# Optimization experiments

Hardware: AMD Instinct MI355X
Metric: run time of the kernel (lower is better)

## Reference

```python
import jax, jax.numpy as jnp
import numpy as np

HEADS = 4

def _layernorm(x, g, b, eps=1e-5):
    mu = x.mean(-1, keepdims=True)
    var = ((x - mu) ** 2).mean(-1, keepdims=True)
    return (x - mu) / jnp.sqrt(var + eps) * g + b

def _feature_map(data, proj, is_query, eps=1e-4):
    # FAVOR+ softmax kernel features. data: [B,H,S,dh], proj: [m,dh]
    dh = data.shape[-1]
    m = proj.shape[0]
    dn = dh ** -0.25
    ratio = m ** -0.5
    dash = jnp.einsum('bhsd,md->bhsm', data * dn, proj)
    diag = 0.5 * jnp.sum((data * dn) ** 2, axis=-1, keepdims=True)
    mx = jnp.max(dash, axis=-1, keepdims=True) if is_query else jnp.max(dash)
    return ratio * (jnp.exp(dash - diag - mx) + eps)

def _causal_linear_attention(q, k, v):
    # q,k: [B,H,S,m] kernel features; v: [B,H,S,dh]
    k_cum = jnp.cumsum(k, axis=2)                                  # [B,H,S,m]
    d_inv = 1.0 / jnp.einsum('bhsm,bhsm->bhs', q, k_cum)           # [B,H,S]
    ctx = jnp.cumsum(jnp.einsum('bhsm,bhsd->bhsmd', k, v), axis=2) # [B,H,S,m,dh]
    return jnp.einsum('bhsmd,bhsm,bhs->bhsd', ctx, q, d_inv)

def reference(x, pre_w, pre_b, ln1_g, ln1_b, wq, wk, wv, wo, bo, proj,
              ln2_g, ln2_b, ff_w1, ff_b1, ff_w2, ff_b2, tgt_w, tgt_b, rd_w, rd_b):
    # preproc: 1x1x1 conv3d + softplus
    xbn = jax.nn.softplus(jnp.einsum('bcthw,oc->bothw', x, pre_w)
                          + pre_b[None, :, None, None, None])
    B, D, T, H, W = xbn.shape
    tokens = xbn.reshape(B, -1, D)  # raw torch-style reshape, S = T*H*W
    S = tokens.shape[1]

    # Performer block (depth=1): prenorm attention + prenorm FF, residuals
    h = _layernorm(tokens, ln1_g, ln1_b)
    split = lambda t: t.reshape(B, S, HEADS, -1).transpose(0, 2, 1, 3)
    q, k, v = split(h @ wq), split(h @ wk), split(h @ wv)
    qp = _feature_map(q, proj, True)
    kp = _feature_map(k, proj, False)
    attn = _causal_linear_attention(qp, kp, v)
    attn = attn.transpose(0, 2, 1, 3).reshape(B, S, D)
    tokens = tokens + attn @ wo + bo
    h2 = _layernorm(tokens, ln2_g, ln2_b)
    tokens = tokens + jax.nn.gelu(h2 @ ff_w1 + ff_b1, approximate=False) @ ff_w2 + ff_b2

    # readout
    out = tokens.reshape(B, D, T, H, W).mean(axis=2)               # [B,D,H,W]
    out = jnp.concatenate([out, x[:, 2, 0][:, None]], axis=1)      # [B,D+1,H,W]
    out = jax.lax.conv_general_dilated(out, tgt_w, (1, 1), [(2, 2), (2, 2)],
                                       dimension_numbers=('NCHW', 'OIHW', 'NCHW'))
    out = out + tgt_b[None, :, None, None]
    out = out.mean(axis=(2, 3))                                    # global avg pool -> [B,1]
    return out @ rd_w.T + rd_b


def setup_inputs() -> dict:
    key = jax.random.key(0)
    ks = jax.random.split(key, 12)
    B, T, H, W = 2, 8, 48, 48
    D, DH, M, FF = 64, 16, 32, 256
    s = lambda k, shape, sc=1.0: jax.random.normal(k, shape, jnp.float32) * sc
    inv = 1.0 / np.sqrt(D)
    return {
        'x': s(ks[0], (B, 3, T, H, W)),
        'pre_w': s(ks[1], (D, 3), 1.0 / np.sqrt(3)),
        'pre_b': jnp.zeros((D,), jnp.float32),
        'ln1_g': jnp.ones((D,), jnp.float32), 'ln1_b': jnp.zeros((D,), jnp.float32),
        'wq': s(ks[2], (D, D), inv), 'wk': s(ks[3], (D, D), inv), 'wv': s(ks[4], (D, D), inv),
        'wo': s(ks[5], (D, D), inv), 'bo': jnp.zeros((D,), jnp.float32),
        'proj': s(ks[6], (M, DH)),
        'ln2_g': jnp.ones((D,), jnp.float32), 'ln2_b': jnp.zeros((D,), jnp.float32),
        'ff_w1': s(ks[7], (D, FF), inv), 'ff_b1': jnp.zeros((FF,), jnp.float32),
        'ff_w2': s(ks[8], (FF, D), 1.0 / np.sqrt(FF)), 'ff_b2': jnp.zeros((D,), jnp.float32),
        'tgt_w': s(ks[9], (1, D + 1, 5, 5), 1.0 / np.sqrt((D + 1) * 25)),
        'tgt_b': jnp.zeros((1,), jnp.float32),
        'rd_w': s(ks[10], (1, 1)), 'rd_b': jnp.zeros((1,), jnp.float32),
    }
```

## Files before the change

### kernel.cpp

```cpp
#include <hip/hip_runtime.h>
#include <hip/hip_bf16.h>
#include <math.h>

typedef __hip_bfloat16 bf16;
typedef __attribute__((ext_vector_type(8))) short short8;
typedef __attribute__((ext_vector_type(16))) float floatx16;

constexpr int B_   = 2;
constexpr int T_   = 8;
constexpr int HW   = 48 * 48;
constexpr int S_   = T_ * HW;
constexpr int D_   = 64;
constexpr int NH   = 4;
constexpr int DH   = 16;
constexpr int M_   = 32;
constexpr int BS   = B_ * S_;
constexpr int BSD  = BS * D_;
constexpr int BH   = B_ * NH;
constexpr int BHS  = BH * S_;
constexpr int CHUNK = 32;
constexpr int NC   = S_ / CHUNK;
constexpr int STATE = M_ * DH + M_;
constexpr int GSLOTS = 64;
constexpr int GSTRIDE = 32;
constexpr int SRG = 16;
constexpr int SRUN = NC / SRG;
constexpr int SCB = 16;
constexpr float DN = 0.5f;
constexpr float RATIO = 0.17677669529663687f;

__device__ __forceinline__ unsigned short f2bf(float f) {
  bf16 h = __float2bfloat16(f);
  return *reinterpret_cast<unsigned short*>(&h);
}
__device__ __forceinline__ float bf2f(bf16 v) { return __bfloat162float(v); }
__device__ __forceinline__ float bfs2f(short s) {
  return __uint_as_float(((unsigned)(unsigned short)s) << 16);
}
__device__ __forceinline__ void atomicMaxFloat(float* addr, float val) {
  if (val >= 0.f) atomicMax((int*)addr, __float_as_int(val));
  else atomicMin((unsigned int*)addr, __float_as_uint(val));
}

__global__ void __launch_bounds__(256) k_prep(const float* __restrict__ wq,
        const float* __restrict__ wk, const float* __restrict__ wv,
        const float* __restrict__ wo, const float* __restrict__ w1,
        const float* __restrict__ proj,
        short* __restrict__ wqT, short* __restrict__ wkT, short* __restrict__ wvT,
        short* __restrict__ woT, short* __restrict__ w1T, short* __restrict__ projb,
        float* __restrict__ gmax) {
  int tid = blockIdx.x * 256 + threadIdx.x;
  if (tid < GSLOTS) ((unsigned*)gmax)[tid * GSTRIDE] = 0xff800000u;
  if (tid < 512) projb[tid] = (short)f2bf(proj[tid]);
  if (tid < 4096) {
    int c = tid >> 6, r = tid & 63;
    wqT[tid] = (short)f2bf(wq[r * 64 + c]);
    wkT[tid] = (short)f2bf(wk[r * 64 + c]);
    wvT[tid] = (short)f2bf(wv[r * 64 + c]);
    woT[tid] = (short)f2bf(wo[r * 64 + c]);
  }
  {
    int c = tid >> 6, r = tid & 63;
    w1T[tid] = (short)f2bf(w1[r * 256 + c]);
  }
}

__global__ void __launch_bounds__(256) k_preqkv(const float* __restrict__ x,
                      const float* __restrict__ pw, const float* __restrict__ pb,
                      const float* __restrict__ g, const float* __restrict__ bb,
                      const short* __restrict__ wqT, const short* __restrict__ wkT,
                      const short* __restrict__ wvT, const short* __restrict__ projb,
                      bf16* __restrict__ tok, bf16* __restrict__ q,
                      bf16* __restrict__ k, bf16* __restrict__ v,
                      float* __restrict__ gmax) {
  __shared__ __align__(16) short sh[32 * 64];
  __shared__ __align__(16) short sk[32 * 64];
  int tid = threadIdx.x;
  int tbase = blockIdx.x * 32;

  {
    size_t f0 = (size_t)tbase * 64;
    int b = (int)(f0 / ((size_t)D_ * S_));
    int rem = (int)(f0 % ((size_t)D_ * S_));
    int d = rem / S_;
    int pos0 = rem % S_;
    float w0 = pw[d * 3 + 0], w1 = pw[d * 3 + 1], w2 = pw[d * 3 + 2], pbd = pb[d];
    const float* xb = x + ((size_t)b * 3) * S_ + pos0 + tid * 8;
    float4 x0a = *(const float4*)(xb);
    float4 x0b = *(const float4*)(xb + 4);
    float4 x1a = *(const float4*)(xb + S_);
    float4 x1b = *(const float4*)(xb + S_ + 4);
    float4 x2a = *(const float4*)(xb + 2 * S_);
    float4 x2b = *(const float4*)(xb + 2 * S_ + 4);
    float xf0[8] = {x0a.x, x0a.y, x0a.z, x0a.w, x0b.x, x0b.y, x0b.z, x0b.w};
    float xf1[8] = {x1a.x, x1a.y, x1a.z, x1a.w, x1b.x, x1b.y, x1b.z, x1b.w};
    float xf2[8] = {x2a.x, x2a.y, x2a.z, x2a.w, x2b.x, x2b.y, x2b.z, x2b.w};
    float t[8];
    short8 tv;
#pragma unroll
    for (int j = 0; j < 8; ++j) {
      float a = xf0[j] * w0 + xf1[j] * w1 + xf2[j] * w2 + pbd;
      t[j] = fmaxf(a, 0.f) + log1pf(expf(-fabsf(a)));
      tv[j] = (short)f2bf(t[j]);
    }
    *(short8*)(tok + f0 + (size_t)tid * 8) = tv;
    float s1 = 0.f, s2 = 0.f;
#pragma unroll
    for (int j = 0; j < 8; ++j) { s1 += t[j]; s2 += t[j] * t[j]; }
#pragma unroll
    for (int off = 4; off; off >>= 1) {
      s1 += __shfl_xor(s1, off, 8);
      s2 += __shfl_xor(s2, off, 8);
    }
    float mu = s1 * (1.f / 64.f);
    float var = s2 * (1.f / 64.f) - mu * mu;
    float rs = rsqrtf(var + 1e-5f);
    int tt = tid >> 3, j8 = tid & 7;
    short8 hv;
#pragma unroll
    for (int j = 0; j < 8; ++j) {
      int c = j8 * 8 + j;
      hv[j] = (short)f2bf((t[j] - mu) * rs * g[c] + bb[c]);
    }
    *(short8*)&sh[tt * 64 + ((j8 ^ (tt & 7)) * 8)] = hv;
  }
  __syncthreads();

  int w = tid >> 6;
  int L = tid & 63;
  int half = L >> 5;
  int n = L & 31;

  if (w < 3) {
    const short* wmT = (w == 0) ? wqT : (w == 1) ? wkT : wvT;
    bf16* outm = (w == 0) ? q : (w == 1) ? k : v;

    short8 a[4];
#pragma unroll
    for (int c = 0; c < 4; ++c)
      a[c] = *(const short8*)&sh[n * 64 + (((c * 2 + half) ^ (n & 7)) * 8)];
#pragma unroll
    for (int ct = 0; ct < 2; ++ct) {
      int col = ct * 32 + n;
      short8 bfrag[4];
#pragma unroll
      for (int c = 0; c < 4; ++c)
        bfrag[c] = *(const short8*)&wmT[col * 64 + c * 16 + half * 8];
      floatx16 acc;
#pragma unroll
      for (int i = 0; i < 16; ++i) acc[i] = 0.f;
      acc = __builtin_amdgcn_mfma_f32_32x32x16_bf16(a[0], bfrag[0], acc, 0, 0, 0);
      acc = __builtin_amdgcn_mfma_f32_32x32x16_bf16(a[1], bfrag[1], acc, 0, 0, 0);
      acc = __builtin_amdgcn_mfma_f32_32x32x16_bf16(a[2], bfrag[2], acc, 0, 0, 0);
      acc = __builtin_amdgcn_mfma_f32_32x32x16_bf16(a[3], bfrag[3], acc, 0, 0, 0);
      int head = col >> 4, di = col & 15;
#pragma unroll
      for (int r = 0; r < 16; ++r) {
        int row = (r & 3) + 8 * (r >> 2) + 4 * half;
        int token = tbase + row;
        int b = token / S_, s = token % S_;
        unsigned short us = f2bf(acc[r]);
        if (w == 2) {
          outm[((size_t)(b * NH + head) * S_ + s) * DH + di] = *(bf16*)&us;
        } else {
          unsigned short usd = f2bf(bfs2f((short)us) * DN);
          outm[((size_t)(b * NH + head) * S_ + s) * DH + di] = *(bf16*)&usd;
          if (w == 1)
            *(short*)((char*)sk + row * 128 + ((col * 2) ^ ((row & 7) << 4))) = (short)usd;
        }
      }
    }
  }
  __syncthreads();

  {
    short8 ak;
    short8 bp = *(const short8*)&projb[n * 16 + half * 8];
    int roff = n * 128 + ((w * 32 + half * 16) ^ ((n & 7) << 4));
    ak = *(const short8*)((const char*)sk + roff);
    floatx16 Pk;
#pragma unroll
    for (int i = 0; i < 16; ++i) Pk[i] = 0.f;
    Pk = __builtin_amdgcn_mfma_f32_32x32x16_bf16(ak, bp, Pk, 0, 0, 0);
    float bmax = -3.4e38f;
#pragma unroll
    for (int r = 0; r < 16; ++r) bmax = fmaxf(bmax, Pk[r]);
    for (int off = 32; off; off >>= 1) bmax = fmaxf(bmax, __shfl_xor(bmax, off));
    if (L == 0)
      atomicMaxFloat(&gmax[((blockIdx.x * 4 + w) & (GSLOTS - 1)) * GSTRIDE], bmax);
  }
}

__global__ void __launch_bounds__(256) k_featcsfin(const float* __restrict__ gmax,
                      const bf16* __restrict__ q, const bf16* __restrict__ k,
                      const bf16* __restrict__ v, const short* __restrict__ projb,
                      bf16* __restrict__ qpb, bf16* __restrict__ kpb,
                      float* __restrict__ ckv) {
  __shared__ __align__(16) float sKp[4][CHUNK * 32];
  int tid = threadIdx.x;
  int w = tid >> 6, L = tid & 63, half = L >> 5, n = L & 31;
  short8 bp = *(const short8*)&projb[n * 16 + half * 8];

  if (blockIdx.x >= BH * NC / 4) {
    int fblk = blockIdx.x - BH * NC / 4;
    int rowbase = fblk * 128 + w * 32;
    short8 aq = *(const short8*)(q + (size_t)(rowbase + n) * 16 + half * 8);
    float dq = 0.f;
#pragma unroll
    for (int j = 0; j < 8; ++j) { float f = bfs2f(aq[j]); dq += f * f; }
    dq += __shfl_xor(dq, 32);
    dq *= 0.5f;
    floatx16 Pq;
#pragma unroll
    for (int i = 0; i < 16; ++i) Pq[i] = 0.f;
    Pq = __builtin_amdgcn_mfma_f32_32x32x16_bf16(aq, bp, Pq, 0, 0, 0);
#pragma unroll
    for (int r = 0; r < 16; ++r) {
      int i = (r & 3) + 8 * (r >> 2) + 4 * half;
      float mx = Pq[r];
      for (int off = 16; off; off >>= 1) mx = fmaxf(mx, __shfl_xor(mx, off, 32));
      float dqi = __shfl(dq, i, 64);
      float val = RATIO * (expf(Pq[r] - dqi - mx) + 1e-4f);
      qpb[(size_t)(rowbase + i) * 32 + n] = __float2bfloat16(val);
    }
    return;
  }

  int chunk = blockIdx.x * 4 + w;
  int bh = chunk / NC, c = chunk % NC;
  int base = bh * S_ + c * CHUNK;
  float gm = gmax[L * GSTRIDE];
  for (int off = 32; off; off >>= 1) gm = fmaxf(gm, __shfl_xor(gm, off));
  short8 ak = *(const short8*)(k + (size_t)(base + n) * 16 + half * 8);
  float dk = 0.f;
#pragma unroll
  for (int j = 0; j < 8; ++j) { float f = bfs2f(ak[j]); dk += f * f; }
  dk += __shfl_xor(dk, 32);
  dk *= 0.5f;
  floatx16 Pk;
#pragma unroll
  for (int i = 0; i < 16; ++i) Pk[i] = 0.f;
  Pk = __builtin_amdgcn_mfma_f32_32x32x16_bf16(ak, bp, Pk, 0, 0, 0);
  float* sp = &sKp[w][0];
#pragma unroll
  for (int r = 0; r < 16; ++r) {
    int i = (r & 3) + 8 * (r >> 2) + 4 * half;
    float dgi = __shfl(dk, i, 64);
    sp[i * 32 + n] = RATIO * (expf(Pk[r] - dgi - gm) + 1e-4f);
  }
  short8 a1, a2;
#pragma unroll
  for (int j = 0; j < 8; ++j) {
    a1[j] = (short)f2bf(sp[(half * 8 + j) * 32 + n]);
    a2[j] = (short)f2bf(sp[(16 + half * 8 + j) * 32 + n]);
  }
  const unsigned short one_bf = f2bf(1.f);
  short8 vb1, vb2;
#pragma unroll
  for (int j = 0; j < 8; ++j) {
    int t1 = half * 8 + j, t2 = 16 + half * 8 + j;
    vb1[j] = (n < 16) ? *(const short*)(v + (size_t)(base + t1) * 16 + n)
                      : (short)(n == 16 ? one_bf : 0);
    vb2[j] = (n < 16) ? *(const short*)(v + (size_t)(base + t2) * 16 + n)
                      : (short)(n == 16 ? one_bf : 0);
  }
  floatx16 O;
#pragma unroll
  for (int i = 0; i < 16; ++i) O[i] = 0.f;
  O = __builtin_amdgcn_mfma_f32_32x32x16_bf16(a1, vb1, O, 0, 0, 0);
  O = __builtin_amdgcn_mfma_f32_32x32x16_bf16(a2, vb2, O, 0, 0, 0);
  float* outp = ckv + (size_t)chunk * STATE;
#pragma unroll
  for (int r = 0; r < 16; ++r) {
    int m = (r & 3) + 8 * (r >> 2) + 4 * half;
    if (n < 16) outp[m * 16 + n] = O[r];
    else if (n == 16) outp[512 + m] = O[r];
  }
  {
    int row = L >> 1, c8 = (L & 1) * 16;
    const float* srcp = sp + row * 32 + c8;
    uint4 u0, u1;
    u0.x = (unsigned)f2bf(srcp[0])  | ((unsigned)f2bf(srcp[1])  << 16);
    u0.y = (unsigned)f2bf(srcp[2])  | ((unsigned)f2bf(srcp[3])  << 16);
    u0.z = (unsigned)f2bf(srcp[4])  | ((unsigned)f2bf(srcp[5])  << 16);
    u0.w = (unsigned)f2bf(srcp[6])  | ((unsigned)f2bf(srcp[7])  << 16);
    u1.x = (unsigned)f2bf(srcp[8])  | ((unsigned)f2bf(srcp[9])  << 16);
    u1.y = (unsigned)f2bf(srcp[10]) | ((unsigned)f2bf(srcp[11]) << 16);
    u1.z = (unsigned)f2bf(srcp[12]) | ((unsigned)f2bf(srcp[13]) << 16);
    u1.w = (unsigned)f2bf(srcp[14]) | ((unsigned)f2bf(srcp[15]) << 16);
    *(uint4*)&kpb[(size_t)(base + row) * 32 + c8] = u0;
    *(uint4*)&kpb[(size_t)(base + row) * 32 + c8 + 8] = u1;
  }
}

__global__ void __launch_bounds__(256) k_scan(float* __restrict__ ckv) {
  __shared__ float sS[SRG][SCB];
  int blk = blockIdx.x;
  int bh = blk / (STATE / SCB);
  int c0 = (blk % (STATE / SCB)) * SCB;
  int cl = threadIdx.x & (SCB - 1);
  int rg = threadIdx.x >> 4;
  int c = c0 + cl;
  size_t base = ((size_t)bh * NC + rg * SRUN) * STATE + c;
  float s = 0.f;
#pragma unroll 6
  for (int i = 0; i < SRUN; ++i) s += ckv[base + (size_t)i * STATE];
  sS[rg][cl] = s;
  __syncthreads();
  float run = 0.f;
  for (int r = 0; r < rg; ++r) run += sS[r][cl];
  for (int i0 = 0; i0 < SRUN; i0 += 6) {
    float tb[6];
#pragma unroll
    for (int j = 0; j < 6; ++j) tb[j] = ckv[base + (size_t)(i0 + j) * STATE];
#pragma unroll
    for (int j = 0; j < 6; ++j) {
      ckv[base + (size_t)(i0 + j) * STATE] = run;
      run += tb[j];
    }
  }
}

__global__ void __launch_bounds__(256) k_attn(const bf16* __restrict__ qpb,
                                              const bf16* __restrict__ kpb,
                                              const bf16* __restrict__ v,
                                              const float* __restrict__ ckv,
                                              bf16* __restrict__ attn) {
  __shared__ __align__(16) float sP[4][32 * 33 + 4];
  int tid = threadIdx.x;
  int w = tid >> 6;
  int L = tid & 63;
  int half = L >> 5;
  int n = L & 31;
  int chunk = blockIdx.x * 4 + w;
  int bh = chunk / NC, c = chunk % NC;
  int base = bh * S_ + c * CHUNK;

  short8 a1 = *(const short8*)(qpb + (size_t)(base + n) * 32 + half * 8);
  short8 a2 = *(const short8*)(qpb + (size_t)(base + n) * 32 + 16 + half * 8);
  short8 b1 = *(const short8*)(kpb + (size_t)(base + n) * 32 + half * 8);
  short8 b2 = *(const short8*)(kpb + (size_t)(base + n) * 32 + 16 + half * 8);

  floatx16 P;
#pragma unroll
  for (int i = 0; i < 16; ++i) P[i] = 0.f;
  P = __builtin_amdgcn_mfma_f32_32x32x16_bf16(a1, b1, P, 0, 0, 0);
  P = __builtin_amdgcn_mfma_f32_32x32x16_bf16(a2, b2, P, 0, 0, 0);

  float* sp = &sP[w][0];
#pragma unroll
  for (int r = 0; r < 16; ++r) {
    int i = (r & 3) + 8 * (r >> 2) + 4 * half;
    sp[i * 33 + n] = (n <= i) ? P[r] : 0.f;
  }
  short8 pa1, pa2;
#pragma unroll
  for (int j = 0; j < 8; ++j) {
    pa1[j] = (short)f2bf(sp[n * 33 + half * 8 + j]);
    pa2[j] = (short)f2bf(sp[n * 33 + 16 + half * 8 + j]);
  }

  const float* cs = ckv + (size_t)chunk * STATE;
  const unsigned short one_bf = f2bf(1.f);
  short8 vb1, vb2, sb1, sb2;
#pragma unroll
  for (int j = 0; j < 8; ++j) {
    int t1 = half * 8 + j, t2 = 16 + half * 8 + j;
    vb1[j] = (n < 16) ? *(const short*)(v + (size_t)(base + t1) * 16 + n)
                      : (short)(n == 16 ? one_bf : 0);
    vb2[j] = (n < 16) ? *(const short*)(v + (size_t)(base + t2) * 16 + n)
                      : (short)(n == 16 ? one_bf : 0);
    float y1 = (n < 16) ? cs[t1 * 16 + n] : (n == 16 ? cs[512 + t1] : 0.f);
    float y2 = (n < 16) ? cs[t2 * 16 + n] : (n == 16 ? cs[512 + t2] : 0.f);
    sb1[j] = (short)f2bf(y1);
    sb2[j] = (short)f2bf(y2);
  }

  floatx16 O;
#pragma unroll
  for (int i = 0; i < 16; ++i) O[i] = 0.f;
  O = __builtin_amdgcn_mfma_f32_32x32x16_bf16(pa1, vb1, O, 0, 0, 0);
  O = __builtin_amdgcn_mfma_f32_32x32x16_bf16(pa2, vb2, O, 0, 0, 0);
  O = __builtin_amdgcn_mfma_f32_32x32x16_bf16(a1, sb1, O, 0, 0, 0);
  O = __builtin_amdgcn_mfma_f32_32x32x16_bf16(a2, sb2, O, 0, 0, 0);

  int srcl = 16 + 32 * half;
  float res[16];
#pragma unroll
  for (int r = 0; r < 16; ++r) {
    float den = __shfl(O[r], srcl, 64);
    res[r] = O[r] / den;
  }
  if (n < 16) {
    int b = bh >> 2, head = bh & 3;
#pragma unroll
    for (int r = 0; r < 16; ++r) {
      int i = (r & 3) + 8 * (r >> 2) + 4 * half;
      attn[((size_t)(b * S_ + c * CHUNK + i)) * 64 + head * 16 + n] = __float2bfloat16(res[r]);
    }
  }
}

__global__ void __launch_bounds__(128) k_wo_ln(const bf16* __restrict__ attn,
                        const short* __restrict__ woT, const float* __restrict__ bo,
                        const bf16* __restrict__ tok, const float* __restrict__ g,
                        const float* __restrict__ bb,
                        bf16* __restrict__ tok2, bf16* __restrict__ h2) {
  __shared__ __align__(16) float sC[32 * 68];
  int tid = threadIdx.x;
  int w = tid >> 6;
  int L = tid & 63;
  int half = L >> 5;
  int n = L & 31;
  int tbase = blockIdx.x * 32;

  short8 a[4];
  {
    const bf16* arow = attn + (size_t)(tbase + n) * 64 + half * 8;
#pragma unroll
    for (int c = 0; c < 4; ++c) a[c] = *(const short8*)(arow + c * 16);
  }
  int col = w * 32 + n;
  short8 bfrag[4];
#pragma unroll
  for (int c = 0; c < 4; ++c)
    bfrag[c] = *(const short8*)&woT[col * 64 + c * 16 + half * 8];
  floatx16 acc;
#pragma unroll
  for (int i = 0; i < 16; ++i) acc[i] = 0.f;
  acc = __builtin_amdgcn_mfma_f32_32x32x16_bf16(a[0], bfrag[0], acc, 0, 0, 0);
  acc = __builtin_amdgcn_mfma_f32_32x32x16_bf16(a[1], bfrag[1], acc, 0, 0, 0);
  acc = __builtin_amdgcn_mfma_f32_32x32x16_bf16(a[2], bfrag[2], acc, 0, 0, 0);
  acc = __builtin_amdgcn_mfma_f32_32x32x16_bf16(a[3], bfrag[3], acc, 0, 0, 0);
  float bias = bo[col];
#pragma unroll
  for (int r = 0; r < 16; ++r) {
    int row = (r & 3) + 8 * (r >> 2) + 4 * half;
    sC[row * 68 + col] = acc[r] + bf2f(tok[(size_t)(tbase + row) * 64 + col]) + bias;
  }
  __syncthreads();
  int tg = tid >> 5, cg = tid & 31;
  int c0 = cg * 2, c1 = c0 + 1;
  float g0 = g[c0], g1 = g[c1], be0 = bb[c0], be1 = bb[c1];
#pragma unroll
  for (int i = 0; i < 8; ++i) {
    int lrow = tg * 8 + i;
    int token = tbase + lrow;
    float t0 = sC[lrow * 68 + c0];
    float t1 = sC[lrow * 68 + c1];
    float s1 = t0 + t1, s2 = t0 * t0 + t1 * t1;
    for (int off = 16; off; off >>= 1) {
      s1 += __shfl_xor(s1, off, 32);
      s2 += __shfl_xor(s2, off, 32);
    }
    float mu = s1 * (1.f / 64.f);
    float var = s2 * (1.f / 64.f) - mu * mu;
    float rs = rsqrtf(var + 1e-5f);
    tok2[token * 64 + c0] = __float2bfloat16(t0);
    tok2[token * 64 + c1] = __float2bfloat16(t1);
    h2[token * 64 + c0] = __float2bfloat16((t0 - mu) * rs * g0 + be0);
    h2[token * 64 + c1] = __float2bfloat16((t1 - mu) * rs * g1 + be1);
  }
}

__global__ void __launch_bounds__(256) k_ffg(const bf16* __restrict__ h2,
                                             const short* __restrict__ w1T,
                                             const float* __restrict__ b1,
                                             float* __restrict__ Gavg) {
  int tid = threadIdx.x;
  int w = tid >> 6;
  int L = tid & 63;
  int half = L >> 5;
  int n = L & 31;
  int blk = blockIdx.x;
  int b = blk / 576;
  int rem = blk % 576;
  int ch = rem / 9;
  int jp0 = (rem % 9) * 4;
  int token_n = b * 18432 + ch * 288 + (n & 7) * 36 + jp0 + (n >> 3);

  short8 a[4];
  {
    const bf16* hrow = h2 + (size_t)token_n * 64 + half * 8;
#pragma unroll
    for (int c = 0; c < 4; ++c) a[c] = *(const short8*)(hrow + c * 16);
  }
  size_t gbase = ((size_t)(b * 64 + ch) * 36 + jp0);
#pragma unroll
  for (int ct = 0; ct < 2; ++ct) {
    int col = w * 64 + ct * 32 + n;
    short8 bfrag[4];
#pragma unroll
    for (int c = 0; c < 4; ++c)
      bfrag[c] = *(const short8*)&w1T[col * 64 + c * 16 + half * 8];
    floatx16 acc;
#pragma unroll
    for (int i = 0; i < 16; ++i) acc[i] = 0.f;
    acc = __builtin_amdgcn_mfma_f32_32x32x16_bf16(a[0], bfrag[0], acc, 0, 0, 0);
    acc = __builtin_amdgcn_mfma_f32_32x32x16_bf16(a[1], bfrag[1], acc, 0, 0, 0);
    acc = __builtin_amdgcn_mfma_f32_32x32x16_bf16(a[2], bfrag[2], acc, 0, 0, 0);
    acc = __builtin_amdgcn_mfma_f32_32x32x16_bf16(a[3], bfrag[3], acc, 0, 0, 0);
    float bias = b1[col];
#pragma unroll
    for (int j = 0; j < 4; ++j) {
      float s = 0.f;
#pragma unroll
      for (int rr = 0; rr < 4; ++rr) {
        float xg = acc[j * 4 + rr] + bias;
        s += 0.5f * xg * (1.f + erff(xg * 0.70710678118654752f));
      }
      s += __shfl_xor(s, 32);
      if (half == 0)
        Gavg[(gbase + j) * 256 + col] = s * 0.125f;
    }
  }
}

__global__ void __launch_bounds__(256) k_pool2(const float* __restrict__ Gavg,
                        const bf16* __restrict__ tok2, const float* __restrict__ w2,
                        const float* __restrict__ b2, float* __restrict__ pool) {
  __shared__ __align__(16) float sG[18 * 256];
  __shared__ __align__(16) float sRed[4 * 18 * 64];
  int blk = blockIdx.x;
  int b = blk / 128;
  int rem = blk % 128;
  int ch = rem >> 1, jph = rem & 1;
  int tid = threadIdx.x;
  size_t grow0 = ((size_t)(b * 64 + ch) * 36 + jph * 18) * 256;
  for (int e = tid; e < 1152; e += 256) {
    int row = e >> 6, c4 = e & 63;
    *(float4*)&sG[row * 256 + c4 * 4] = *(const float4*)&Gavg[grow0 + row * 256 + c4 * 4];
  }
  __syncthreads();
  int kg = tid >> 6, dd = tid & 63;
  float acc[18];
#pragma unroll
  for (int i = 0; i < 18; ++i) acc[i] = 0.f;
  for (int k4 = 0; k4 < 16; ++k4) {
    int k = kg * 64 + k4 * 4;
    float w0 = w2[(k + 0) * 64 + dd];
    float w1 = w2[(k + 1) * 64 + dd];
    float w2v = w2[(k + 2) * 64 + dd];
    float w3 = w2[(k + 3) * 64 + dd];
#pragma unroll
    for (int i = 0; i < 18; ++i) {
      float4 gf = *(const float4*)&sG[i * 256 + k];
      acc[i] += gf.x * w0 + gf.y * w1 + gf.z * w2v + gf.w * w3;
    }
  }
#pragma unroll
  for (int i = 0; i < 18; ++i) sRed[(kg * 18 + i) * 64 + dd] = acc[i];
  __syncthreads();
  for (int o = tid; o < 1152; o += 256) {
    int jp18 = o >> 6, d2 = o & 63;
    float gsum = sRed[(0 * 18 + jp18) * 64 + d2] + sRed[(1 * 18 + jp18) * 64 + d2]
               + sRed[(2 * 18 + jp18) * 64 + d2] + sRed[(3 * 18 + jp18) * 64 + d2];
    int p = (jph * 18 + jp18) * 64 + d2;
    size_t tbase = (size_t)b * 1179648 + (size_t)ch * 18432 + p;
    float ts = 0.f;
#pragma unroll
    for (int t = 0; t < 8; ++t) ts += bf2f(tok2[tbase + t * 2304]);
    pool[((size_t)(b * 64 + ch)) * HW + p] = ts * 0.125f + gsum + b2[d2];
  }
}

__global__ void __launch_bounds__(256) k_convsum(const float* __restrict__ pool,
                                                 const float* __restrict__ x,
                                                 const float* __restrict__ w,
                                                 float* __restrict__ partial) {
  int blk = blockIdx.x;
  int b = blk / 65, ch = blk % 65;
  int tid = threadIdx.x;
  __shared__ float cls[25];
  __shared__ float red[256];
  if (tid < 25) {
    int ry = tid / 5, rx = tid % 5;
    int kh0 = (ry <= 2) ? 0 : (ry == 3 ? 1 : 2);
    int kh1 = (ry >= 2) ? 4 : (ry == 1 ? 3 : 2);
    int kw0 = (rx <= 2) ? 0 : (rx == 3 ? 1 : 2);
    int kw1 = (rx >= 2) ? 4 : (rx == 1 ? 3 : 2);
    float s = 0.f;
    for (int kh = kh0; kh <= kh1; ++kh)
      for (int kw = kw0; kw <= kw1; ++kw)
        s += w[ch * 25 + kh * 5 + kw];
    cls[tid] = s;
  }
  __syncthreads();
  const float* pc = (ch < 64) ? (pool + ((size_t)(b * 64 + ch)) * HW)
                              : (x + (size_t)b * 3 * S_ + 2 * S_);
  float acc = 0.f;
#pragma unroll
  for (int e = tid; e < HW; e += 256) {
    int iy = e / 48, ix = e % 48;
    int ry = (iy == 0) ? 0 : (iy == 1) ? 1 : (iy <= 45) ? 2 : (iy == 46) ? 3 : 4;
    int rx = (ix == 0) ? 0 : (ix == 1) ? 1 : (ix <= 45) ? 2 : (ix == 46) ? 3 : 4;
    acc += pc[e] * cls[ry * 5 + rx];
  }
  red[tid] = acc;
  __syncthreads();
  for (int s = 128; s; s >>= 1) {
    if (tid < s) red[tid] += red[tid + s];
    __syncthreads();
  }
  if (!tid) partial[blk] = red[0];
}

__global__ void k_final(const float* __restrict__ partial, const float* __restrict__ tgt_b,
                        const float* __restrict__ rd_w, const float* __restrict__ rd_b,
                        float* __restrict__ out) {
  int b = blockIdx.x;
  int lane = threadIdx.x;
  float s = (lane < 65) ? partial[b * 65 + lane] : 0.f;
  for (int off = 32; off; off >>= 1) s += __shfl_down(s, off, 64);
  __shared__ float r2;
  if (lane == 64) r2 = s;
  __syncthreads();
  if (!lane) {
    float tot = s + r2;
    float mean = tot / 2304.f + tgt_b[0];
    out[b] = mean * rd_w[0] + rd_b[0];
  }
}

extern "C" void kernel_launch(void* const* d_in, const int* in_sizes, int n_in,
                              void* d_out, int out_size, void* d_ws, size_t ws_size,
                              hipStream_t stream) {
  const float* x     = (const float*)d_in[0];
  const float* pre_w = (const float*)d_in[1];
  const float* pre_b = (const float*)d_in[2];
  const float* ln1_g = (const float*)d_in[3];
  const float* ln1_b = (const float*)d_in[4];
  const float* wq    = (const float*)d_in[5];
  const float* wk    = (const float*)d_in[6];
  const float* wv    = (const float*)d_in[7];
  const float* wo    = (const float*)d_in[8];
  const float* bo    = (const float*)d_in[9];
  const float* proj  = (const float*)d_in[10];
  const float* ln2_g = (const float*)d_in[11];
  const float* ln2_b = (const float*)d_in[12];
  const float* ff_w1 = (const float*)d_in[13];
  const float* ff_b1 = (const float*)d_in[14];
  const float* ff_w2 = (const float*)d_in[15];
  const float* ff_b2 = (const float*)d_in[16];
  const float* tgt_w = (const float*)d_in[17];
  const float* tgt_b = (const float*)d_in[18];
  const float* rd_w  = (const float*)d_in[19];
  const float* rd_b  = (const float*)d_in[20];
  float* out = (float*)d_out;

  float* ws = (float*)d_ws;
  bf16*  tok   = (bf16*)ws;
  bf16*  v     = (bf16*)(ws + (size_t)BSD);
  bf16*  q     = (bf16*)(ws + 2 * (size_t)BSD);
  float* Gavg  = ws + 2 * (size_t)BSD;
  float* pool  = Gavg + 1179648;
  bf16*  k     = (bf16*)(ws + 3 * (size_t)BSD);
  bf16*  h2    = (bf16*)(ws + 4 * (size_t)BSD);
  bf16*  qpb   = (bf16*)(ws + 6 * (size_t)BSD);
  bf16*  kpb   = (bf16*)(ws + 7 * (size_t)BSD);
  float* ckv   = ws + 8 * (size_t)BSD;
  bf16*  tok2  = (bf16*)(ws + 8 * (size_t)BSD);
  bf16*  attnb = k;
  float* smalls = ws + 9 * (size_t)BSD + 147456;
  float* gmax  = smalls;
  float* partial = smalls + 2048;
  short* wqT   = (short*)(smalls + 2304);
  short* wkT   = (short*)(smalls + 4352);
  short* wvT   = (short*)(smalls + 6400);
  short* woT   = (short*)(smalls + 8448);
  short* w1T   = (short*)(smalls + 10496);
  short* projb = (short*)(smalls + 18688);

  k_prep<<<dim3(64), dim3(256), 0, stream>>>(wq, wk, wv, wo, ff_w1, proj,
                                             wqT, wkT, wvT, woT, w1T, projb, gmax);
  k_preqkv<<<dim3(BS / 32), dim3(256), 0, stream>>>(x, pre_w, pre_b, ln1_g, ln1_b,
                                                    wqT, wkT, wvT, projb, tok, q, k, v, gmax);
  k_featcsfin<<<dim3(BH * NC / 4 + BHS / 128), dim3(256), 0, stream>>>(gmax, q, k, v, projb,
                                                                       qpb, kpb, ckv);
  k_scan<<<dim3(BH * (STATE / SCB)), dim3(256), 0, stream>>>(ckv);
  k_attn<<<dim3(BH * NC / 4), dim3(256), 0, stream>>>(qpb, kpb, v, ckv, attnb);
  k_wo_ln<<<dim3(BS / 32), dim3(128), 0, stream>>>(attnb, woT, bo, tok, ln2_g, ln2_b, tok2, h2);
  k_ffg<<<dim3(B_ * 64 * 9), dim3(256), 0, stream>>>(h2, w1T, ff_b1, Gavg);
  k_pool2<<<dim3(B_ * 64 * 2), dim3(256), 0, stream>>>(Gavg, tok2, ff_w2, ff_b2, pool);
  k_convsum<<<dim3(B_ * 65), dim3(256), 0, stream>>>(pool, x, tgt_w, partial);
  k_final<<<dim3(B_), dim3(128), 0, stream>>>(partial, tgt_b, rd_w, rd_b, out);
}
```

Before: 197.8 us.

## Fuse causal attention with output projection and LayerNorm; drop sync in key-max

The attention kernel now handles all four heads of a token chunk in one block. It stages the per-head outputs in swizzled shared memory and applies the Wo projection, residual and LayerNorm in place, so the separate k_wo_ln kernel and the global round-trip of the attention output are gone. In k_preqkv, a single wave computes the key-feature max over all heads after its own LDS writes, which removes a block-wide barrier and cuts atomic traffic to one per block. The trade-off is that only two of the four waves do the Wo GEMM, and the workspace layout shifts so tok2 no longer aliases ckv.

Measured after the change: 197.5 us. Within noise of the previous version (-0.1%).

```diff
diff --git a/kernel.cpp b/kernel.cpp
--- a/kernel.cpp
+++ b/kernel.cpp
@@ -171,23 +171,24 @@
       }
     }
   }
-  __syncthreads();
-
-  {
-    short8 ak;
+
+  if (w == 1) {
     short8 bp = *(const short8*)&projb[n * 16 + half * 8];
-    int roff = n * 128 + ((w * 32 + half * 16) ^ ((n & 7) << 4));
-    ak = *(const short8*)((const char*)sk + roff);
-    floatx16 Pk;
-#pragma unroll
-    for (int i = 0; i < 16; ++i) Pk[i] = 0.f;
-    Pk = __builtin_amdgcn_mfma_f32_32x32x16_bf16(ak, bp, Pk, 0, 0, 0);
     float bmax = -3.4e38f;
 #pragma unroll
-    for (int r = 0; r < 16; ++r) bmax = fmaxf(bmax, Pk[r]);
+    for (int h = 0; h < 4; ++h) {
+      int roff = n * 128 + ((h * 32 + half * 16) ^ ((n & 7) << 4));
+      short8 ak = *(const short8*)((const char*)sk + roff);
+      floatx16 Pk;
+#pragma unroll
+      for (int i = 0; i < 16; ++i) Pk[i] = 0.f;
+      Pk = __builtin_amdgcn_mfma_f32_32x32x16_bf16(ak, bp, Pk, 0, 0, 0);
+#pragma unroll
+      for (int r = 0; r < 16; ++r) bmax = fmaxf(bmax, Pk[r]);
+    }
     for (int off = 32; off; off >>= 1) bmax = fmaxf(bmax, __shfl_xor(bmax, off));
     if (L == 0)
-      atomicMaxFloat(&gmax[((blockIdx.x * 4 + w) & (GSLOTS - 1)) * GSTRIDE], bmax);
+      atomicMaxFloat(&gmax[(blockIdx.x & (GSLOTS - 1)) * GSTRIDE], bmax);
   }
 }
 
@@ -321,20 +322,26 @@
   }
 }
 
-__global__ void __launch_bounds__(256) k_attn(const bf16* __restrict__ qpb,
-                                              const bf16* __restrict__ kpb,
-                                              const bf16* __restrict__ v,
-                                              const float* __restrict__ ckv,
-                                              bf16* __restrict__ attn) {
+__global__ void __launch_bounds__(256) k_attnwo(const bf16* __restrict__ qpb,
+                        const bf16* __restrict__ kpb, const bf16* __restrict__ v,
+                        const float* __restrict__ ckv, const short* __restrict__ woT,
+                        const float* __restrict__ bo, const bf16* __restrict__ tok,
+                        const float* __restrict__ g, const float* __restrict__ bb,
+                        bf16* __restrict__ tok2, bf16* __restrict__ h2) {
   __shared__ __align__(16) float sP[4][32 * 33 + 4];
+  __shared__ __align__(16) short sA[32 * 64];
+  __shared__ __align__(16) float sC[32 * 68];
   int tid = threadIdx.x;
   int w = tid >> 6;
   int L = tid & 63;
   int half = L >> 5;
   int n = L & 31;
-  int chunk = blockIdx.x * 4 + w;
-  int bh = chunk / NC, c = chunk % NC;
+  int blk = blockIdx.x;
+  int b = blk / NC, c = blk % NC;
+  int bh = b * NH + w;
   int base = bh * S_ + c * CHUNK;
+  int chunk = bh * NC + c;
+  int tbase = b * S_ + c * CHUNK;
 
   short8 a1 = *(const short8*)(qpb + (size_t)(base + n) * 32 + half * 8);
   short8 a2 = *(const short8*)(qpb + (size_t)(base + n) * 32 + 16 + half * 8);
@@ -392,59 +399,46 @@
     res[r] = O[r] / den;
   }
   if (n < 16) {
-    int b = bh >> 2, head = bh & 3;
 #pragma unroll
     for (int r = 0; r < 16; ++r) {
       int i = (r & 3) + 8 * (r >> 2) + 4 * half;
-      attn[((size_t)(b * S_ + c * CHUNK + i)) * 64 + head * 16 + n] = __float2bfloat16(res[r]);
-    }
-  }
-}
-
-__global__ void __launch_bounds__(128) k_wo_ln(const bf16* __restrict__ attn,
-                        const short* __restrict__ woT, const float* __restrict__ bo,
-                        const bf16* __restrict__ tok, const float* __restrict__ g,
-                        const float* __restrict__ bb,
-                        bf16* __restrict__ tok2, bf16* __restrict__ h2) {
-  __shared__ __align__(16) float sC[32 * 68];
-  int tid = threadIdx.x;
-  int w = tid >> 6;
-  int L = tid & 63;
-  int half = L >> 5;
-  int n = L & 31;
-  int tbase = blockIdx.x * 32;
-
-  short8 a[4];
-  {
-    const bf16* arow = attn + (size_t)(tbase + n) * 64 + half * 8;
-#pragma unroll
-    for (int c = 0; c < 4; ++c) a[c] = *(const short8*)(arow + c * 16);
-  }
-  int col = w * 32 + n;
-  short8 bfrag[4];
-#pragma unroll
-  for (int c = 0; c < 4; ++c)
-    bfrag[c] = *(const short8*)&woT[col * 64 + c * 16 + half * 8];
-  floatx16 acc;
-#pragma unroll
-  for (int i = 0; i < 16; ++i) acc[i] = 0.f;
-  acc = __builtin_amdgcn_mfma_f32_32x32x16_bf16(a[0], bfrag[0], acc, 0, 0, 0);
-  acc = __builtin_amdgcn_mfma_f32_32x32x16_bf16(a[1], bfrag[1], acc, 0, 0, 0);
-  acc = __builtin_amdgcn_mfma_f32_32x32x16_bf16(a[2], bfrag[2], acc, 0, 0, 0);
-  acc = __builtin_amdgcn_mfma_f32_32x32x16_bf16(a[3], bfrag[3], acc, 0, 0, 0);
-  float bias = bo[col];
-#pragma unroll
-  for (int r = 0; r < 16; ++r) {
-    int row = (r & 3) + 8 * (r >> 2) + 4 * half;
-    sC[row * 68 + col] = acc[r] + bf2f(tok[(size_t)(tbase + row) * 64 + col]) + bias;
-  }
-  __syncthreads();
+      sA[i * 64 + (((w * 2 + (n >> 3)) ^ (i & 7)) << 3) + (n & 7)] = (short)f2bf(res[r]);
+    }
+  }
+  __syncthreads();
+
+  if (w < 2) {
+    short8 a[4];
+#pragma unroll
+    for (int cdx = 0; cdx < 4; ++cdx)
+      a[cdx] = *(const short8*)&sA[n * 64 + (((cdx * 2 + half) ^ (n & 7)) * 8)];
+    int col = w * 32 + n;
+    short8 bfrag[4];
+#pragma unroll
+    for (int cdx = 0; cdx < 4; ++cdx)
+      bfrag[cdx] = *(const short8*)&woT[col * 64 + cdx * 16 + half * 8];
+    floatx16 acc;
+#pragma unroll
+    for (int i = 0; i < 16; ++i) acc[i] = 0.f;
+    acc = __builtin_amdgcn_mfma_f32_32x32x16_bf16(a[0], bfrag[0], acc, 0, 0, 0);
+    acc = __builtin_amdgcn_mfma_f32_32x32x16_bf16(a[1], bfrag[1], acc, 0, 0, 0);
+    acc = __builtin_amdgcn_mfma_f32_32x32x16_bf16(a[2], bfrag[2], acc, 0, 0, 0);
+    acc = __builtin_amdgcn_mfma_f32_32x32x16_bf16(a[3], bfrag[3], acc, 0, 0, 0);
+    float bias = bo[col];
+#pragma unroll
+    for (int r = 0; r < 16; ++r) {
+      int row = (r & 3) + 8 * (r >> 2) + 4 * half;
+      sC[row * 68 + col] = acc[r] + bf2f(tok[(size_t)(tbase + row) * 64 + col]) + bias;
+    }
+  }
+  __syncthreads();
+
   int tg = tid >> 5, cg = tid & 31;
   int c0 = cg * 2, c1 = c0 + 1;
   float g0 = g[c0], g1 = g[c1], be0 = bb[c0], be1 = bb[c1];
 #pragma unroll
-  for (int i = 0; i < 8; ++i) {
-    int lrow = tg * 8 + i;
+  for (int i = 0; i < 4; ++i) {
+    int lrow = tg * 4 + i;
     int token = tbase + lrow;
     float t0 = sC[lrow * 68 + c0];
     float t1 = sC[lrow * 68 + c1];
@@ -456,10 +450,10 @@
     float mu = s1 * (1.f / 64.f);
     float var = s2 * (1.f / 64.f) - mu * mu;
     float rs = rsqrtf(var + 1e-5f);
-    tok2[token * 64 + c0] = __float2bfloat16(t0);
-    tok2[token * 64 + c1] = __float2bfloat16(t1);
-    h2[token * 64 + c0] = __float2bfloat16((t0 - mu) * rs * g0 + be0);
-    h2[token * 64 + c1] = __float2bfloat16((t1 - mu) * rs * g1 + be1);
+    tok2[(size_t)token * 64 + c0] = __float2bfloat16(t0);
+    tok2[(size_t)token * 64 + c1] = __float2bfloat16(t1);
+    h2[(size_t)token * 64 + c0] = __float2bfloat16((t0 - mu) * rs * g0 + be0);
+    h2[(size_t)token * 64 + c1] = __float2bfloat16((t1 - mu) * rs * g1 + be1);
   }
 }
 
@@ -659,9 +653,8 @@
   bf16*  qpb   = (bf16*)(ws + 6 * (size_t)BSD);
   bf16*  kpb   = (bf16*)(ws + 7 * (size_t)BSD);
   float* ckv   = ws + 8 * (size_t)BSD;
-  bf16*  tok2  = (bf16*)(ws + 8 * (size_t)BSD);
-  bf16*  attnb = k;
-  float* smalls = ws + 9 * (size_t)BSD + 147456;
+  bf16*  tok2  = (bf16*)(ws + 8 * (size_t)BSD + 2506752);
+  float* smalls = ws + 9 * (size_t)BSD + 147456 + 2506752;
   float* gmax  = smalls;
   float* partial = smalls + 2048;
   short* wqT   = (short*)(smalls + 2304);
@@ -678,8 +671,8 @@
   k_featcsfin<<<dim3(BH * NC / 4 + BHS / 128), dim3(256), 0, stream>>>(gmax, q, k, v, projb,
                                                                        qpb, kpb, ckv);
   k_scan<<<dim3(BH * (STATE / SCB)), dim3(256), 0, stream>>>(ckv);
-  k_attn<<<dim3(BH * NC / 4), dim3(256), 0, stream>>>(qpb, kpb, v, ckv, attnb);
-  k_wo_ln<<<dim3(BS / 32), dim3(128), 0, stream>>>(attnb, woT, bo, tok, ln2_g, ln2_b, tok2, h2);
+  k_attnwo<<<dim3(B_ * NC), dim3(256), 0, stream>>>(qpb, kpb, v, ckv, woT, bo, tok,
+                                                    ln2_g, ln2_b, tok2, h2);
   k_ffg<<<dim3(B_ * 64 * 9), dim3(256), 0, stream>>>(h2, w1T, ff_b1, Gavg);
   k_pool2<<<dim3(B_ * 64 * 2), dim3(256), 0, stream>>>(Gavg, tok2, ff_w2, ff_b2, pool);
   k_convsum<<<dim3(B_ * 65), dim3(256), 0, stream>>>(pool, x, tgt_w, partial);
```
